# Kernel optimization log

Hardware: AMD Instinct MI355X
Metric: run time of the kernel (lower is better)

Reference implementation:

```python
import jax, jax.numpy as jnp
import numpy as np

B, D, E, H, O, TOP_K = 65536, 256, 16, 256, 256, 2
GATE_T = 1.0  # gate_temperature default


def setup_inputs() -> dict:
    key = jax.random.key(0)
    ks = jax.random.split(key, 8)
    sn = lambda k, shape, sc: (jax.random.normal(k, shape, jnp.float32) * sc)
    return {
        "x": sn(ks[0], (B, D), 1.0),
        # per-expert input bias, init N(0, 0.02) as in the module
        "bias": sn(ks[1], (E, D), 0.02),
        # expert MLP params: Linear(D,H) -> ReLU -> Linear(H,O), stacked over experts
        "W1": sn(ks[2], (E, D, H), 1.0 / np.sqrt(D)),
        "b1": jnp.zeros((E, H), jnp.float32),
        "W2": sn(ks[3], (E, H, O), 1.0 / np.sqrt(H)),
        "b2": jnp.zeros((E, O), jnp.float32),
        # gate MLP: Linear(D,4D) -> ReLU -> Linear(4D,D) -> ReLU -> Linear(D,E)
        "g1": sn(ks[4], (D, 4 * D), 1.0 / np.sqrt(D)),
        "gb1": jnp.zeros((4 * D,), jnp.float32),
        "g2": sn(ks[5], (4 * D, D), 1.0 / np.sqrt(4 * D)),
        "gb2": jnp.zeros((D,), jnp.float32),
        "g3": sn(ks[6], (D, E), 1.0 / np.sqrt(D)),
        "gb3": jnp.zeros((E,), jnp.float32),
    }


def reference(x, bias, W1, b1, W2, b2, g1, gb1, g2, gb2, g3, gb3):
    # --- gate ---
    h = jax.nn.relu(x @ g1 + gb1)
    h = jax.nn.relu(h @ g2 + gb2)
    gate_logits = h @ g3 + gb3              # [B, E]
    T = max(GATE_T, 1e-6)
    p = jax.nn.softmax(gate_logits / T, axis=1)

    # --- top-k sparsification + renormalize (top_k < num_experts) ---
    topv, topi = jax.lax.top_k(p, TOP_K)    # [B, K]
    rows = jnp.arange(p.shape[0])[:, None]
    p_sparse = jnp.zeros_like(p).at[rows, topi].set(topv)
    p = p_sparse / (p_sparse.sum(axis=1, keepdims=True) + 1e-9)

    # --- dense all-experts compute (module runs every expert on every token) ---
    xb = x[:, None, :] + bias[None]                                  # [B, E, D]
    he = jax.nn.relu(jnp.einsum("bed,edh->beh", xb, W1) + b1)      # [B, E, H]
    outs_all = jnp.einsum("beh,eho->beo", he, W2) + b2             # [B, E, O]

    # --- weighted combine (stopgrad_gate=False -> grads flow through p) ---
    y = jnp.einsum("be,beo->bo", p, outs_all)                      # [B, O]
    return (y, p)
```

## Files before the change

### kernel.cpp

```cpp
#include <hip/hip_runtime.h>
#include <cstdint>
#include <cstddef>

#define BTOK 65536
#define DDIM 256
#define NEXP 16
#define HDIM 256
#define ODIM 256
#define TAU2 1.2e-2f
#define TAU3 1.2e-4
#define AMB2_CAP 12288
#define AMB3_CAP 1024
#define LCAP (BTOK + 2048)

typedef _Float16 fp16x8 __attribute__((ext_vector_type(8)));
typedef float    f32x4_t __attribute__((ext_vector_type(4)));

__device__ __forceinline__ void async_ld16(const void* g, void* l) {
  __builtin_amdgcn_global_load_lds(
      (const __attribute__((address_space(1))) unsigned int*)g,
      (__attribute__((address_space(3))) unsigned int*)l, 16, 0, 0);
}

__global__ __launch_bounds__(256) void k_transpose_cvt(
    const float* __restrict__ src, _Float16* __restrict__ dhi,
    _Float16* __restrict__ dlo, int R, int C) {
  __shared__ float s[32][33];
  int bz = blockIdx.z;
  size_t stride = (size_t)R * C;
  src += (size_t)bz * stride;
  dhi += (size_t)bz * stride;
  if (dlo) dlo += (size_t)bz * stride;
  int c0 = blockIdx.x * 32, r0 = blockIdx.y * 32;
  int tx = threadIdx.x & 31, ty = threadIdx.x >> 5;
  for (int k = 0; k < 32; k += 8)
    s[ty + k][tx] = src[(size_t)(r0 + ty + k) * C + c0 + tx];
  __syncthreads();
  for (int k = 0; k < 32; k += 8) {
    float v = s[tx][ty + k];
    _Float16 h = (_Float16)v;
    size_t o = (size_t)(c0 + ty + k) * R + r0 + tx;
    dhi[o] = h;
    if (dlo) dlo[o] = (_Float16)(v - (float)h);
  }
}

__global__ __launch_bounds__(256) void k_xcvt_hi(const float* __restrict__ x,
                                                 _Float16* __restrict__ xhi, int n8) {
  int i = blockIdx.x * 256 + threadIdx.x;
  if (i >= n8) return;
  const float4* p = (const float4*)x;
  float4 a = p[(size_t)i * 2], b = p[(size_t)i * 2 + 1];
  float v[8] = {a.x, a.y, a.z, a.w, b.x, b.y, b.z, b.w};
  fp16x8 hv;
#pragma unroll
  for (int j = 0; j < 8; j++) hv[j] = (_Float16)v[j];
  *(fp16x8*)(xhi + (size_t)i * 8) = hv;
}

__global__ __launch_bounds__(256) void k_gemm_f16(
    const _Float16* __restrict__ A, const _Float16* __restrict__ B,
    const float* __restrict__ bias, _Float16* __restrict__ C,
    int M, int N, int K) {
  __shared__ _Float16 sA[128 * 32], sB[128 * 32];
  const int tid = threadIdx.x;
  const int lane = tid & 63;
  const int wave = tid >> 6;
  const int wr = wave >> 1, wc = wave & 1;
  const int m0 = blockIdx.y * 128, n0 = blockIdx.x * 128;
  f32x4_t zero4 = {0.f, 0.f, 0.f, 0.f};
  f32x4_t acc[4][4];
#pragma unroll
  for (int i = 0; i < 4; i++)
#pragma unroll
    for (int j = 0; j < 4; j++) acc[i][j] = zero4;

  for (int k0 = 0; k0 < K; k0 += 32) {
#pragma unroll
    for (int r = 0; r < 2; r++) {
      int idx = r * 256 + tid;
      int row = idx >> 2, ch = idx & 3;
      int gch = ch ^ (row & 3);
      async_ld16(A + (size_t)(m0 + row) * K + k0 + gch * 8, &sA[idx * 8]);
      async_ld16(B + (size_t)(n0 + row) * K + k0 + gch * 8, &sB[idx * 8]);
    }
    __syncthreads();
    fp16x8 a[4], b[4];
    int kc = lane >> 4;
#pragma unroll
    for (int i = 0; i < 4; i++) {
      int ar = wr * 64 + i * 16 + (lane & 15);
      a[i] = *(const fp16x8*)&sA[ar * 32 + ((kc ^ (ar & 3)) << 3)];
      int br = wc * 64 + i * 16 + (lane & 15);
      b[i] = *(const fp16x8*)&sB[br * 32 + ((kc ^ (br & 3)) << 3)];
    }
#pragma unroll
    for (int i = 0; i < 4; i++)
#pragma unroll
      for (int j = 0; j < 4; j++)
        acc[i][j] = __builtin_amdgcn_mfma_f32_16x16x32_f16(a[i], b[j], acc[i][j], 0, 0, 0);
    __syncthreads();
  }
#pragma unroll
  for (int j = 0; j < 4; j++) {
    int col = n0 + wc * 64 + j * 16 + (lane & 15);
    float bc = bias[col];
#pragma unroll
    for (int i = 0; i < 4; i++)
#pragma unroll
      for (int q = 0; q < 4; q++) {
        int row = m0 + wr * 64 + i * 16 + ((lane >> 4) << 2) + q;
        float v = acc[i][j][q] + bc;
        v = v > 0.f ? v : 0.f;
        C[(size_t)row * N + col] = (_Float16)v;
      }
  }
}

__global__ __launch_bounds__(256) void k_gemm_split(
    const _Float16* __restrict__ Ahi, const _Float16* __restrict__ Alo,
    const _Float16* __restrict__ Bhi, const _Float16* __restrict__ Blo,
    const float* __restrict__ bias,
    _Float16* __restrict__ Chi, _Float16* __restrict__ Clo,
    int M, int N, int K, const int* __restrict__ nAct) {
  int nA = *nAct;
  if (nA > M) nA = M;
  const int m0 = blockIdx.y * 128, n0 = blockIdx.x * 128;
  if (m0 >= nA) return;
  __shared__ _Float16 sAh[128 * 32], sAl[128 * 32], sBh[128 * 32], sBl[128 * 32];
  const int tid = threadIdx.x;
  const int lane = tid & 63;
  const int wave = tid >> 6;
  const int wr = wave >> 1, wc = wave & 1;
  f32x4_t zero4 = {0.f, 0.f, 0.f, 0.f};
  f32x4_t acc[4][4];
#pragma unroll
  for (int i = 0; i < 4; i++)
#pragma unroll
    for (int j = 0; j < 4; j++) acc[i][j] = zero4;

  for (int k0 = 0; k0 < K; k0 += 32) {
#pragma unroll
    for (int r = 0; r < 2; r++) {
      int idx = r * 256 + tid;
      int row = idx >> 2, ch = idx & 3;
      int gch = ch ^ (row & 3);
      size_t ga = (size_t)(m0 + row) * K + k0 + gch * 8;
      size_t gb = (size_t)(n0 + row) * K + k0 + gch * 8;
      async_ld16(Ahi + ga, &sAh[idx * 8]);
      async_ld16(Alo + ga, &sAl[idx * 8]);
      async_ld16(Bhi + gb, &sBh[idx * 8]);
      async_ld16(Blo + gb, &sBl[idx * 8]);
    }
    __syncthreads();
    fp16x8 ah[4], al[4], bh[4], bl[4];
    int kc = lane >> 4;
#pragma unroll
    for (int i = 0; i < 4; i++) {
      int ar = wr * 64 + i * 16 + (lane & 15);
      int offa = ar * 32 + ((kc ^ (ar & 3)) << 3);
      ah[i] = *(const fp16x8*)&sAh[offa];
      al[i] = *(const fp16x8*)&sAl[offa];
      int br = wc * 64 + i * 16 + (lane & 15);
      int offb = br * 32 + ((kc ^ (br & 3)) << 3);
      bh[i] = *(const fp16x8*)&sBh[offb];
      bl[i] = *(const fp16x8*)&sBl[offb];
    }
#pragma unroll
    for (int i = 0; i < 4; i++)
#pragma unroll
      for (int j = 0; j < 4; j++) {
        acc[i][j] = __builtin_amdgcn_mfma_f32_16x16x32_f16(ah[i], bh[j], acc[i][j], 0, 0, 0);
        acc[i][j] = __builtin_amdgcn_mfma_f32_16x16x32_f16(ah[i], bl[j], acc[i][j], 0, 0, 0);
        acc[i][j] = __builtin_amdgcn_mfma_f32_16x16x32_f16(al[i], bh[j], acc[i][j], 0, 0, 0);
      }
    __syncthreads();
  }
#pragma unroll
  for (int j = 0; j < 4; j++) {
    int col = n0 + wc * 64 + j * 16 + (lane & 15);
    float bc = bias[col];
#pragma unroll
    for (int i = 0; i < 4; i++)
#pragma unroll
      for (int q = 0; q < 4; q++) {
        int row = m0 + wr * 64 + i * 16 + ((lane >> 4) << 2) + q;
        float v = acc[i][j][q] + bc;
        v = v > 0.f ? v : 0.f;
        _Float16 h = (_Float16)v;
        size_t o = (size_t)row * N + col;
        Chi[o] = h;
        Clo[o] = (_Float16)(v - (float)h);
      }
  }
}

__global__ __launch_bounds__(256) void k_gate3_fast(
    const _Float16* __restrict__ h2h, const float* __restrict__ g3,
    const float* __restrict__ gb3,
    float* __restrict__ pout, int* __restrict__ idx0, int* __restrict__ idx1,
    float* __restrict__ w0, float* __restrict__ w1,
    int* __restrict__ amb2Cnt, int* __restrict__ amb2List,
    int* __restrict__ cnt0, int* __restrict__ cnt1) {
  __shared__ _Float16 shh[16 * 256];
  __shared__ float sg3[16][260];
  __shared__ float sgb[16];
  __shared__ float slog[16][17];
  __shared__ int sidx[16][2];
  __shared__ float swv[16][2];
  __shared__ int hc0[16], hc1[16];
  int tid = threadIdx.x;
  int tokBase = blockIdx.x * 16;
  if (tid < 16) { hc0[tid] = 0; hc1[tid] = 0; }
  {
    int t = tid >> 4, c = (tid & 15) * 16;
    size_t g = (size_t)(tokBase + t) * 256 + c;
    *(fp16x8*)&shh[t * 256 + c] = *(const fp16x8*)&h2h[g];
    *(fp16x8*)&shh[t * 256 + c + 8] = *(const fp16x8*)&h2h[g + 8];
  }
#pragma unroll
  for (int r = 0; r < 16; r++) {
    int j = r * 256 + tid;
    sg3[j & 15][j >> 4] = g3[j];
  }
  if (tid < 16) sgb[tid] = gb3[tid];
  __syncthreads();
  int t = tid >> 4, e = tid & 15;
  const _Float16* ph = &shh[t * 256];
  const float* pg = &sg3[e][0];
  float acc = 0.f;
  for (int k = 0; k < 256; k += 8) {
    fp16x8 hv = *(const fp16x8*)&ph[k];
    float4 ga = *(const float4*)&pg[k];
    float4 gb = *(const float4*)&pg[k + 4];
    acc = fmaf((float)hv[0], ga.x, acc);
    acc = fmaf((float)hv[1], ga.y, acc);
    acc = fmaf((float)hv[2], ga.z, acc);
    acc = fmaf((float)hv[3], ga.w, acc);
    acc = fmaf((float)hv[4], gb.x, acc);
    acc = fmaf((float)hv[5], gb.y, acc);
    acc = fmaf((float)hv[6], gb.z, acc);
    acc = fmaf((float)hv[7], gb.w, acc);
  }
  acc += sgb[e];
  slog[t][e] = acc;
  __syncthreads();
  if (e == 0) {
    float l[16];
#pragma unroll
    for (int i = 0; i < 16; i++) l[i] = slog[t][i];
    int i1 = 0;
    for (int i = 1; i < 16; i++) if (l[i] > l[i1]) i1 = i;
    int i2 = -1;
    for (int i = 0; i < 16; i++) { if (i == i1) continue; if (i2 < 0 || l[i] > l[i2]) i2 = i; }
    float l3 = -1e30f;
    for (int i = 0; i < 16; i++) { if (i == i1 || i == i2) continue; if (l[i] > l3) l3 = l[i]; }
    float lmax = l[i1];
    float S = 0.f;
    for (int i = 0; i < 16; i++) S += expf(l[i] - lmax);
    float p1 = 1.0f / S, p2 = expf(l[i2] - lmax) / S;
    float den = p1 + p2 + 1e-9f;
    sidx[t][0] = i1; sidx[t][1] = i2;
    swv[t][0] = p1 / den; swv[t][1] = p2 / den;
    atomicAdd(&hc0[i1], 1);
    atomicAdd(&hc1[i2], 1);
    if (l[i2] - l3 < TAU2) {
      int pos = atomicAdd(amb2Cnt, 1);
      if (pos < AMB2_CAP) amb2List[pos] = tokBase + t;
    }
  }
  __syncthreads();
  int i1 = sidx[t][0], i2 = sidx[t][1];
  float pv = (e == i1) ? swv[t][0] : ((e == i2) ? swv[t][1] : 0.f);
  pout[(size_t)(tokBase + t) * 16 + e] = pv;
  if (e == 0) {
    int tok = tokBase + t;
    idx0[tok] = i1; idx1[tok] = i2;
    w0[tok] = swv[t][0]; w1[tok] = swv[t][1];
  }
  if (tid < 16) {
    if (hc0[tid]) atomicAdd(&cnt0[tid], hc0[tid]);
    if (hc1[tid]) atomicAdd(&cnt1[tid], hc1[tid]);
  }
}

__global__ __launch_bounds__(256) void k_gather2(
    const float* __restrict__ x, const int* __restrict__ cnt,
    const int* __restrict__ list,
    _Float16* __restrict__ xgh, _Float16* __restrict__ xgl) {
  int n = *cnt; if (n > AMB2_CAP) n = AMB2_CAP;
  int s = blockIdx.x * 8 + (threadIdx.x >> 5);
  if (s >= n) return;
  int tok = list[s];
  int c = (threadIdx.x & 31) * 8;
  const float4* p = (const float4*)&x[(size_t)tok * 256 + c];
  float4 a = p[0], b = p[1];
  float v[8] = {a.x, a.y, a.z, a.w, b.x, b.y, b.z, b.w};
  fp16x8 hv, lv;
#pragma unroll
  for (int j = 0; j < 8; j++) {
    _Float16 h = (_Float16)v[j];
    hv[j] = h;
    lv[j] = (_Float16)(v[j] - (float)h);
  }
  *(fp16x8*)&xgh[(size_t)s * 256 + c] = hv;
  *(fp16x8*)&xgl[(size_t)s * 256 + c] = lv;
}

__global__ __launch_bounds__(256) void k_gate3_precise(
    const _Float16* __restrict__ h2ghi, const _Float16* __restrict__ h2glo,
    const float* __restrict__ g3, const float* __restrict__ gb3,
    const int* __restrict__ amb2Cnt, const int* __restrict__ amb2List,
    float* __restrict__ pout, int* __restrict__ idx0, int* __restrict__ idx1,
    float* __restrict__ w0, float* __restrict__ w1,
    int* __restrict__ amb3Cnt, int* __restrict__ amb3List,
    int* __restrict__ cnt0, int* __restrict__ cnt1) {
  __shared__ _Float16 shh[16 * 256], shl[16 * 256];
  __shared__ float sg3[16][260];
  __shared__ float sgb[16];
  __shared__ double slog[16][17];
  __shared__ int sidx[16][2];
  __shared__ float swv[16][2];
  int tid = threadIdx.x;
  int slotBase = blockIdx.x * 16;
  int n2 = *amb2Cnt; if (n2 > AMB2_CAP) n2 = AMB2_CAP;
  {
    int t = tid >> 4, c = (tid & 15) * 16;
    size_t g = (size_t)(slotBase + t) * 256 + c;
    *(fp16x8*)&shh[t * 256 + c] = *(const fp16x8*)&h2ghi[g];
    *(fp16x8*)&shh[t * 256 + c + 8] = *(const fp16x8*)&h2ghi[g + 8];
    *(fp16x8*)&shl[t * 256 + c] = *(const fp16x8*)&h2glo[g];
    *(fp16x8*)&shl[t * 256 + c + 8] = *(const fp16x8*)&h2glo[g + 8];
  }
#pragma unroll
  for (int r = 0; r < 16; r++) {
    int j = r * 256 + tid;
    sg3[j & 15][j >> 4] = g3[j];
  }
  if (tid < 16) sgb[tid] = gb3[tid];
  __syncthreads();
  int t = tid >> 4, e = tid & 15;
  int slot = slotBase + t;
  const _Float16* ph = &shh[t * 256];
  const _Float16* pl = &shl[t * 256];
  const float* pg = &sg3[e][0];
  double acc = 0.0;
  for (int k = 0; k < 256; k += 4) {
#pragma unroll
    for (int j = 0; j < 4; j++) {
      double a = (double)(float)ph[k + j] + (double)(float)pl[k + j];
      acc = fma(a, (double)pg[k + j], acc);
    }
  }
  acc += (double)sgb[e];
  slog[t][e] = acc;
  __syncthreads();
  if (e == 0 && slot < n2) {
    int tok = amb2List[slot];
    double l[16];
#pragma unroll
    for (int i = 0; i < 16; i++) l[i] = slog[t][i];
    int i1 = 0;
    for (int i = 1; i < 16; i++) if (l[i] > l[i1]) i1 = i;
    int i2 = -1;
    for (int i = 0; i < 16; i++) { if (i == i1) continue; if (i2 < 0 || l[i] > l[i2]) i2 = i; }
    double l3 = -1e300;
    for (int i = 0; i < 16; i++) { if (i == i1 || i == i2) continue; if (l[i] > l3) l3 = l[i]; }
    double lmax = l[i1];
    double S = 0.0;
    for (int i = 0; i < 16; i++) S += exp(l[i] - lmax);
    double p1 = 1.0 / S, p2 = exp(l[i2] - lmax) / S;
    double den = p1 + p2 + 1e-9;
    sidx[t][0] = i1; sidx[t][1] = i2;
    swv[t][0] = (float)(p1 / den); swv[t][1] = (float)(p2 / den);
    int o0 = idx0[tok], o1 = idx1[tok];
    if (i1 != o0) { atomicSub(&cnt0[o0], 1); atomicAdd(&cnt0[i1], 1); }
    if (i2 != o1) { atomicSub(&cnt1[o1], 1); atomicAdd(&cnt1[i2], 1); }
    if (l[i2] - l3 < TAU3) {
      int pos = atomicAdd(amb3Cnt, 1);
      if (pos < AMB3_CAP) amb3List[pos] = tok;
    }
  }
  __syncthreads();
  if (slot < n2) {
    int tok = amb2List[slot];
    int i1 = sidx[t][0], i2 = sidx[t][1];
    float pv = (e == i1) ? swv[t][0] : ((e == i2) ? swv[t][1] : 0.f);
    pout[(size_t)tok * 16 + e] = pv;
    if (e == 0) {
      idx0[tok] = i1; idx1[tok] = i2;
      w0[tok] = swv[t][0]; w1[tok] = swv[t][1];
    }
  }
}

__global__ __launch_bounds__(256) void k_ref_l1(
    const float* __restrict__ x, const float* __restrict__ g1,
    const float* __restrict__ gb1,
    const int* __restrict__ cnt, const int* __restrict__ list,
    double* __restrict__ h1d) {
  int n = *cnt; if (n > AMB3_CAP) n = AMB3_CAP;
  int t = blockIdx.y;
  if (t >= n) return;
  __shared__ float sx[256];
  __shared__ double sred[4][64];
  int tid = threadIdx.x;
  int tok = list[t];
  sx[tid] = x[(size_t)tok * 256 + tid];
  __syncthreads();
  int o = tid & 63, p = tid >> 6;
  int out = blockIdx.x * 64 + o;
  double a = 0.0;
  const float* gp = g1 + (size_t)(p * 64) * 1024 + out;
  const float* xp = &sx[p * 64];
#pragma unroll 8
  for (int k = 0; k < 64; k++)
    a = fma((double)xp[k], (double)gp[(size_t)k * 1024], a);
  sred[p][o] = a;
  __syncthreads();
  if (p == 0) {
    double s = sred[0][o] + sred[1][o] + sred[2][o] + sred[3][o] + (double)gb1[out];
    h1d[(size_t)t * 1024 + out] = s > 0.0 ? s : 0.0;
  }
}

__global__ __launch_bounds__(512) void k_ref_l2(
    const double* __restrict__ h1d, const float* __restrict__ g2,
    const float* __restrict__ gb2,
    const int* __restrict__ cnt, double* __restrict__ h2d) {
  int n = *cnt; if (n > AMB3_CAP) n = AMB3_CAP;
  int t = blockIdx.y;
  if (t >= n) return;
  __shared__ double sh1[1024];
  __shared__ double sred[8][64];
  int tid = threadIdx.x;
  sh1[tid] = h1d[(size_t)t * 1024 + tid];
  sh1[512 + tid] = h1d[(size_t)t * 1024 + 512 + tid];
  __syncthreads();
  int o = tid & 63, p = tid >> 6;
  int out = blockIdx.x * 64 + o;
  double a = 0.0;
  const float* gp = g2 + (size_t)(p * 128) * 256 + out;
  const double* hp = &sh1[p * 128];
#pragma unroll 4
  for (int k = 0; k < 128; k++)
    a = fma(hp[k], (double)gp[(size_t)k * 256], a);
  sred[p][o] = a;
  __syncthreads();
  if (p == 0) {
    double s = sred[0][o] + sred[1][o] + sred[2][o] + sred[3][o] +
               sred[4][o] + sred[5][o] + sred[6][o] + sred[7][o] + (double)gb2[out];
    h2d[(size_t)t * 256 + out] = s > 0.0 ? s : 0.0;
  }
}

__global__ __launch_bounds__(256) void k_ref_l3(
    const double* __restrict__ h2d, const float* __restrict__ g3,
    const float* __restrict__ gb3,
    const int* __restrict__ cnt, const int* __restrict__ list,
    float* __restrict__ pout, int* __restrict__ idx0, int* __restrict__ idx1,
    float* __restrict__ w0, float* __restrict__ w1,
    int* __restrict__ cnt0, int* __restrict__ cnt1) {
  int n = *cnt; if (n > AMB3_CAP) n = AMB3_CAP;
  int t = blockIdx.x;
  if (t >= n) return;
  __shared__ double sh2[256];
  __shared__ double sl16[16][17];
  __shared__ int sidx[2];
  __shared__ float swv[2];
  int tid = threadIdx.x;
  int tok = list[t];
  sh2[tid] = h2d[(size_t)t * 256 + tid];
  __syncthreads();
  {
    int o = tid & 15, pp = tid >> 4;
    double a = 0.0;
#pragma unroll
    for (int k = pp * 16; k < pp * 16 + 16; k++)
      a = fma(sh2[k], (double)g3[(size_t)k * 16 + o], a);
    sl16[pp][o] = a;
  }
  __syncthreads();
  if (tid == 0) {
    double l[16];
    for (int o = 0; o < 16; o++) {
      double a = (double)gb3[o];
      for (int p = 0; p < 16; p++) a += sl16[p][o];
      l[o] = a;
    }
    int i1 = 0;
    for (int i = 1; i < 16; i++) if (l[i] > l[i1]) i1 = i;
    int i2 = -1;
    for (int i = 0; i < 16; i++) { if (i == i1) continue; if (i2 < 0 || l[i] > l[i2]) i2 = i; }
    double lmax = l[i1];
    double S = 0.0;
    for (int i = 0; i < 16; i++) S += exp(l[i] - lmax);
    double p1 = 1.0 / S, p2 = exp(l[i2] - lmax) / S;
    double den = p1 + p2 + 1e-9;
    float fw0 = (float)(p1 / den), fw1 = (float)(p2 / den);
    int o0 = idx0[tok], o1 = idx1[tok];
    if (i1 != o0) { atomicSub(&cnt0[o0], 1); atomicAdd(&cnt0[i1], 1); }
    if (i2 != o1) { atomicSub(&cnt1[o1], 1); atomicAdd(&cnt1[i2], 1); }
    sidx[0] = i1; sidx[1] = i2;
    swv[0] = fw0; swv[1] = fw1;
    idx0[tok] = i1; idx1[tok] = i2;
    w0[tok] = fw0; w1[tok] = fw1;
  }
  __syncthreads();
  if (tid < 16) {
    float pv = (tid == sidx[0]) ? swv[0] : ((tid == sidx[1]) ? swv[1] : 0.f);
    pout[(size_t)tok * 16 + tid] = pv;
  }
}

__global__ void k_offsets(const int* __restrict__ cnt0, const int* __restrict__ cnt1,
                          int* off0, int* off1, int* cur0, int* cur1,
                          int* dExpC, int* dRowC, int* nTiles) {
  if (threadIdx.x == 0) {
    int tot = 0, nt = 0;
    for (int e = 0; e < 16; e++) {
      off0[e] = tot; cur0[e] = 0;
      int tiles = (cnt0[e] + 127) >> 7;
      for (int ti = 0; ti < tiles; ti++) { dExpC[nt] = e; dRowC[nt] = tot + ti * 128; nt++; }
      tot += tiles * 128;
    }
    nTiles[0] = nt;
    tot = 0;
    for (int e = 0; e < 16; e++) {
      off1[e] = tot; cur1[e] = 0;
      int tiles = (cnt1[e] + 127) >> 7;
      for (int ti = 0; ti < tiles; ti++) { dExpC[nt] = e; dRowC[nt] = LCAP + tot + ti * 128; nt++; }
      tot += tiles * 128;
    }
    nTiles[1] = nt;
  }
}

__global__ __launch_bounds__(256) void k_scatter(
    const int* __restrict__ idx0, const int* __restrict__ idx1,
    const float* __restrict__ w0, const float* __restrict__ w1,
    const int* __restrict__ off0, const int* __restrict__ off1,
    int* cur0, int* cur1,
    int* __restrict__ tok0, float* __restrict__ wl0,
    int* __restrict__ tok1, float* __restrict__ wl1) {
  __shared__ int c0[16], c1[16], b0[16], b1[16];
  int tid = threadIdx.x;
  if (tid < 16) { c0[tid] = 0; c1[tid] = 0; }
  __syncthreads();
  int b = blockIdx.x * 256 + tid;
  int e0 = idx0[b], e1 = idx1[b];
  int r0 = atomicAdd(&c0[e0], 1);
  int r1 = atomicAdd(&c1[e1], 1);
  __syncthreads();
  if (tid < 16) { b0[tid] = atomicAdd(&cur0[tid], c0[tid]); b1[tid] = atomicAdd(&cur1[tid], c1[tid]); }
  __syncthreads();
  int p0 = off0[e0] + b0[e0] + r0;
  tok0[p0] = b; wl0[p0] = w0[b];
  int p1 = off1[e1] + b1[e1] + r1;
  tok1[p1] = b; wl1[p1] = w1[b];
}

__global__ __launch_bounds__(512) void k_grp_l1(
    const _Float16* __restrict__ xhi, const float* __restrict__ bias,
    const _Float16* __restrict__ W1T, const float* __restrict__ b1,
    const int* __restrict__ tokAll,
    const int* __restrict__ dExp, const int* __restrict__ dRow,
    const int* __restrict__ nT, _Float16* __restrict__ heg) {
  __shared__ _Float16 sA[128 * 32];
  __shared__ _Float16 sB[256 * 32];
  __shared__ int sTok[128];
  __shared__ float sBias[256];
  int tid = threadIdx.x, lane = tid & 63, wave = tid >> 6;
  int wr = wave >> 2, wc = wave & 3;
  f32x4_t zero4 = {0.f, 0.f, 0.f, 0.f};
  int nt = *nT;
  for (int t = blockIdx.x; t < nt; t += gridDim.x) {
    int e = dExp[t], rowOff = dRow[t];
    if (tid < 128) sTok[tid] = tokAll[rowOff + tid];
    if (tid < 256) sBias[tid] = bias[e * 256 + tid];
    __syncthreads();
    f32x4_t acc[4][4];
#pragma unroll
    for (int i = 0; i < 4; i++)
#pragma unroll
      for (int j = 0; j < 4; j++) acc[i][j] = zero4;
    const _Float16* W1e = W1T + (size_t)e * 65536;
    for (int k0 = 0; k0 < 256; k0 += 32) {
      {
        int row = tid >> 2, ch = tid & 3, gch = ch ^ (row & 3);
        int tok = sTok[row];
        int tk = tok < 0 ? 0 : tok;
        fp16x8 v = *(const fp16x8*)&xhi[(size_t)tk * 256 + k0 + gch * 8];
        const float* bp = &sBias[k0 + gch * 8];
#pragma unroll
        for (int j = 0; j < 8; j++) v[j] = (_Float16)((float)v[j] + bp[j]);
        *(fp16x8*)&sA[tid * 8] = v;
      }
#pragma unroll
      for (int r = 0; r < 2; r++) {
        int idx = r * 512 + tid;
        int row = idx >> 2, ch = idx & 3, gch = ch ^ (row & 3);
        async_ld16(W1e + (size_t)row * 256 + k0 + gch * 8, &sB[idx * 8]);
      }
      __syncthreads();
      fp16x8 a[4], b[4];
      int kc = lane >> 4;
#pragma unroll
      for (int i = 0; i < 4; i++) {
        int ar = wr * 64 + i * 16 + (lane & 15);
        a[i] = *(const fp16x8*)&sA[ar * 32 + ((kc ^ (ar & 3)) << 3)];
        int br = wc * 64 + i * 16 + (lane & 15);
        b[i] = *(const fp16x8*)&sB[br * 32 + ((kc ^ (br & 3)) << 3)];
      }
#pragma unroll
      for (int i = 0; i < 4; i++)
#pragma unroll
        for (int j = 0; j < 4; j++)
          acc[i][j] = __builtin_amdgcn_mfma_f32_16x16x32_f16(a[i], b[j], acc[i][j], 0, 0, 0);
      __syncthreads();
    }
#pragma unroll
    for (int j = 0; j < 4; j++) {
      int col = wc * 64 + j * 16 + (lane & 15);
      float bb = b1[e * 256 + col];
#pragma unroll
      for (int i = 0; i < 4; i++)
#pragma unroll
        for (int q = 0; q < 4; q++) {
          int row = wr * 64 + i * 16 + ((lane >> 4) << 2) + q;
          float v = acc[i][j][q] + bb;
          heg[(size_t)(rowOff + row) * 256 + col] = (_Float16)(v > 0.f ? v : 0.f);
        }
    }
    __syncthreads();
  }
}

template <int PASSB>
__global__ __launch_bounds__(512) void k_grp_l2(
    const _Float16* __restrict__ heg, const _Float16* __restrict__ W2T,
    const float* __restrict__ b2,
    const int* __restrict__ tokAll, const float* __restrict__ wlAll,
    const int* __restrict__ dExp, const int* __restrict__ dRow,
    const int* __restrict__ nT0, const int* __restrict__ nTC,
    float* __restrict__ y) {
  __shared__ _Float16 sA[128 * 32];
  __shared__ _Float16 sB[256 * 32];
  __shared__ int sTok[128];
  __shared__ float sW[128];
  int tid = threadIdx.x, lane = tid & 63, wave = tid >> 6;
  int wr = wave >> 2, wc = wave & 3;
  f32x4_t zero4 = {0.f, 0.f, 0.f, 0.f};
  int tStart = PASSB ? *nT0 : 0;
  int tEnd = PASSB ? *nTC : *nT0;
  for (int t = tStart + blockIdx.x; t < tEnd; t += gridDim.x) {
    int e = dExp[t], rowOff = dRow[t];
    if (tid < 128) { sTok[tid] = tokAll[rowOff + tid]; sW[tid] = wlAll[rowOff + tid]; }
    __syncthreads();
    f32x4_t acc[4][4];
#pragma unroll
    for (int i = 0; i < 4; i++)
#pragma unroll
      for (int j = 0; j < 4; j++) acc[i][j] = zero4;
    const _Float16* W2e = W2T + (size_t)e * 65536;
    for (int k0 = 0; k0 < 256; k0 += 32) {
      {
        int row = tid >> 2, ch = tid & 3, gch = ch ^ (row & 3);
        async_ld16(heg + (size_t)(rowOff + row) * 256 + k0 + gch * 8, &sA[tid * 8]);
      }
#pragma unroll
      for (int r = 0; r < 2; r++) {
        int idx = r * 512 + tid;
        int row = idx >> 2, ch = idx & 3, gch = ch ^ (row & 3);
        async_ld16(W2e + (size_t)row * 256 + k0 + gch * 8, &sB[idx * 8]);
      }
      __syncthreads();
      fp16x8 a[4], b[4];
      int kc = lane >> 4;
#pragma unroll
      for (int i = 0; i < 4; i++) {
        int ar = wr * 64 + i * 16 + (lane & 15);
        a[i] = *(const fp16x8*)&sA[ar * 32 + ((kc ^ (ar & 3)) << 3)];
        int br = wc * 64 + i * 16 + (lane & 15);
        b[i] = *(const fp16x8*)&sB[br * 32 + ((kc ^ (br & 3)) << 3)];
      }
#pragma unroll
      for (int i = 0; i < 4; i++)
#pragma unroll
        for (int j = 0; j < 4; j++)
          acc[i][j] = __builtin_amdgcn_mfma_f32_16x16x32_f16(a[i], b[j], acc[i][j], 0, 0, 0);
      __syncthreads();
    }
#pragma unroll
    for (int j = 0; j < 4; j++) {
      int col = wc * 64 + j * 16 + (lane & 15);
      float bb = b2[e * 256 + col];
#pragma unroll
      for (int i = 0; i < 4; i++)
#pragma unroll
        for (int q = 0; q < 4; q++) {
          int row = wr * 64 + i * 16 + ((lane >> 4) << 2) + q;
          int tok = sTok[row];
          if (tok >= 0) {
            float v = (acc[i][j][q] + bb) * sW[row];
            size_t o = (size_t)tok * 256 + col;
            if (PASSB) y[o] += v; else y[o] = v;
          }
        }
    }
    __syncthreads();
  }
}

extern "C" void kernel_launch(void* const* d_in, const int* in_sizes, int n_in,
                              void* d_out, int out_size, void* d_ws, size_t ws_size,
                              hipStream_t stream) {
  const float* x   = (const float*)d_in[0];
  const float* bias= (const float*)d_in[1];
  const float* W1  = (const float*)d_in[2];
  const float* b1  = (const float*)d_in[3];
  const float* W2  = (const float*)d_in[4];
  const float* b2  = (const float*)d_in[5];
  const float* g1  = (const float*)d_in[6];
  const float* gb1 = (const float*)d_in[7];
  const float* g2  = (const float*)d_in[8];
  const float* gb2 = (const float*)d_in[9];
  const float* g3  = (const float*)d_in[10];
  const float* gb3 = (const float*)d_in[11];
  float* y    = (float*)d_out;
  float* pout = y + (size_t)BTOK * 256;

  char* w = (char*)d_ws;
  auto alloc = [&](size_t bytes) -> char* {
    char* p = w;
    w += (bytes + 255) & ~(size_t)255;
    return p;
  };
  _Float16* xhi  = (_Float16*)alloc((size_t)BTOK * 256 * 2);
  _Float16* h2h  = (_Float16*)alloc((size_t)BTOK * 256 * 2);
  _Float16* g1Th = (_Float16*)alloc((size_t)256 * 1024 * 2);
  _Float16* g1Tl = (_Float16*)alloc((size_t)256 * 1024 * 2);
  _Float16* g2Th = (_Float16*)alloc((size_t)256 * 1024 * 2);
  _Float16* g2Tl = (_Float16*)alloc((size_t)256 * 1024 * 2);
  _Float16* W1T  = (_Float16*)alloc((size_t)16 * 65536 * 2);
  _Float16* W2T  = (_Float16*)alloc((size_t)16 * 65536 * 2);
  int*   idx0 = (int*)alloc((size_t)BTOK * 4);
  int*   idx1 = (int*)alloc((size_t)BTOK * 4);
  float* w0a  = (float*)alloc((size_t)BTOK * 4);
  float* w1a  = (float*)alloc((size_t)BTOK * 4);
  int*   ctrl = (int*)alloc(4096);
  int*   amb2List = (int*)alloc((size_t)AMB2_CAP * 4);
  int*   amb3List = (int*)alloc((size_t)AMB3_CAP * 4);
  int*   dExpC = (int*)alloc(1088 * 4);
  int*   dRowC = (int*)alloc(1088 * 4);
  int*   tokAll = (int*)alloc((size_t)2 * LCAP * 4);
  float* wlAll  = (float*)alloc((size_t)2 * LCAP * 4);
  _Float16* xgh  = (_Float16*)alloc((size_t)AMB2_CAP * 256 * 2);
  _Float16* xgl  = (_Float16*)alloc((size_t)AMB2_CAP * 256 * 2);
  _Float16* h1gh = (_Float16*)alloc((size_t)AMB2_CAP * 1024 * 2);
  _Float16* h1gl = (_Float16*)alloc((size_t)AMB2_CAP * 1024 * 2);
  _Float16* h2gh = (_Float16*)alloc((size_t)AMB2_CAP * 256 * 2);
  _Float16* h2gl = (_Float16*)alloc((size_t)AMB2_CAP * 256 * 2);
  _Float16* heg = (_Float16*)xgh;
  double* h1d = (double*)alloc((size_t)AMB3_CAP * 1024 * 8);
  double* h2d = (double*)alloc((size_t)AMB3_CAP * 256 * 8);

  size_t used = (size_t)(w - (char*)d_ws);
  size_t remain = ws_size > used ? ws_size - used : 0;
  int CG = 1;
  while (CG < 64 && (size_t)(BTOK / CG) * 1024 * 2 + 1024 > remain) CG <<= 1;
  int MC = BTOK / CG;
  _Float16* h1h = (_Float16*)alloc((size_t)MC * 1024 * 2);

  int* cnt0 = ctrl + 0;  int* cnt1 = ctrl + 16;
  int* off0 = ctrl + 32; int* off1 = ctrl + 48;
  int* cur0 = ctrl + 64; int* cur1 = ctrl + 80;
  int* nTiles = ctrl + 96;
  int* amb2Cnt = ctrl + 112;
  int* amb3Cnt = ctrl + 116;

  hipMemsetAsync(ctrl, 0, 4096, stream);
  hipMemsetAsync(tokAll, 0xFF, (size_t)2 * LCAP * 4, stream);

  dim3 tb(256);
  k_transpose_cvt<<<dim3(32, 8, 1), tb, 0, stream>>>(g1, g1Th, g1Tl, 256, 1024);
  k_transpose_cvt<<<dim3(8, 32, 1), tb, 0, stream>>>(g2, g2Th, g2Tl, 1024, 256);
  k_transpose_cvt<<<dim3(8, 8, 16), tb, 0, stream>>>(W1, W1T, nullptr, 256, 256);
  k_transpose_cvt<<<dim3(8, 8, 16), tb, 0, stream>>>(W2, W2T, nullptr, 256, 256);
  k_xcvt_hi<<<(BTOK * 256 / 8 + 255) / 256, tb, 0, stream>>>(x, xhi, BTOK * 256 / 8);

  for (int c = 0; c < CG; c++) {
    const _Float16* xh = xhi + (size_t)c * MC * 256;
    k_gemm_f16<<<dim3(8, MC / 128), tb, 0, stream>>>(xh, g1Th, gb1, h1h, MC, 1024, 256);
    k_gemm_f16<<<dim3(2, MC / 128), tb, 0, stream>>>(h1h, g2Th, gb2,
                                                     h2h + (size_t)c * MC * 256, MC, 256, 1024);
  }
  k_gate3_fast<<<BTOK / 16, tb, 0, stream>>>(h2h, g3, gb3, pout, idx0, idx1,
                                             w0a, w1a, amb2Cnt, amb2List, cnt0, cnt1);

  k_gather2<<<AMB2_CAP / 8, tb, 0, stream>>>(x, amb2Cnt, amb2List, xgh, xgl);
  k_gemm_split<<<dim3(8, AMB2_CAP / 128), tb, 0, stream>>>(
      xgh, xgl, g1Th, g1Tl, gb1, h1gh, h1gl, AMB2_CAP, 1024, 256, amb2Cnt);
  k_gemm_split<<<dim3(2, AMB2_CAP / 128), tb, 0, stream>>>(
      h1gh, h1gl, g2Th, g2Tl, gb2, h2gh, h2gl, AMB2_CAP, 256, 1024, amb2Cnt);
  k_gate3_precise<<<AMB2_CAP / 16, tb, 0, stream>>>(
      h2gh, h2gl, g3, gb3, amb2Cnt, amb2List, pout, idx0, idx1, w0a, w1a,
      amb3Cnt, amb3List, cnt0, cnt1);

  k_ref_l1<<<dim3(16, AMB3_CAP), tb, 0, stream>>>(x, g1, gb1, amb3Cnt, amb3List, h1d);
  k_ref_l2<<<dim3(4, AMB3_CAP), 512, 0, stream>>>(h1d, g2, gb2, amb3Cnt, h2d);
  k_ref_l3<<<AMB3_CAP, tb, 0, stream>>>(h2d, g3, gb3, amb3Cnt, amb3List,
                                        pout, idx0, idx1, w0a, w1a, cnt0, cnt1);

  k_offsets<<<1, 64, 0, stream>>>(cnt0, cnt1, off0, off1, cur0, cur1,
                                  dExpC, dRowC, nTiles);
  k_scatter<<<BTOK / 256, tb, 0, stream>>>(idx0, idx1, w0a, w1a, off0, off1,
                                           cur0, cur1, tokAll, wlAll,
                                           tokAll + LCAP, wlAll + LCAP);
  k_grp_l1<<<1056, 512, 0, stream>>>(xhi, bias, W1T, b1, tokAll,
                                     dExpC, dRowC, nTiles + 1, heg);
  k_grp_l2<0><<<528, 512, 0, stream>>>(heg, W2T, b2, tokAll, wlAll,
                                       dExpC, dRowC, nTiles, nTiles + 1, y);
  k_grp_l2<1><<<528, 512, 0, stream>>>(heg, W2T, b2, tokAll, wlAll,
                                       dExpC, dRowC, nTiles, nTiles + 1, y);
}
```

Before: 726.8 us.

## Use MFMA for gate logits, split top-2, and stage expert epilogues through LDS

The scalar FMA gate-3 kernel is replaced by an MFMA 16x16x32 fp16 logits kernel, using g3 converted to fp16, plus a separate one-token-per-thread top-2 kernel that goes through a global logits buffer. The expert layer-1 and layer-2 epilogues now stage outputs in shared memory so each row is written with vectorized, coalesced global stores instead of scattered scalar ones. This trades extra syncthreads and an extra logits round trip for fewer FP32 ALU operations and better store coalescing. Converting g3 to fp16 changes logit precision, which could shift which tokens are flagged as ambiguous and sent through the precise path.

```diff
diff --git a/kernel.cpp b/kernel.cpp
--- a/kernel.cpp
+++ b/kernel.cpp
@@ -43,6 +43,13 @@
     dhi[o] = h;
     if (dlo) dlo[o] = (_Float16)(v - (float)h);
   }
+}
+
+__global__ __launch_bounds__(256) void k_g3cvt(const float* __restrict__ g3,
+                                               _Float16* __restrict__ g3T) {
+  int idx = blockIdx.x * 256 + threadIdx.x;
+  int k = idx >> 4, e = idx & 15;
+  g3T[e * 256 + k] = (_Float16)g3[idx];
 }
 
 __global__ __launch_bounds__(256) void k_xcvt_hi(const float* __restrict__ x,
@@ -195,93 +202,98 @@
   }
 }
 
-__global__ __launch_bounds__(256) void k_gate3_fast(
-    const _Float16* __restrict__ h2h, const float* __restrict__ g3,
-    const float* __restrict__ gb3,
+__global__ __launch_bounds__(256) void k_logits(
+    const _Float16* __restrict__ h2h, const _Float16* __restrict__ g3T,
+    const float* __restrict__ gb3, float* __restrict__ logits) {
+  __shared__ _Float16 sA[128 * 32];
+  __shared__ _Float16 sG[16 * 264];
+  int tid = threadIdx.x, lane = tid & 63, wave = tid >> 6;
+  int m0 = blockIdx.x * 128;
+  {
+    int r = tid >> 4, c = (tid & 15) * 16;
+    *(fp16x8*)&sG[r * 264 + c]     = *(const fp16x8*)&g3T[r * 256 + c];
+    *(fp16x8*)&sG[r * 264 + c + 8] = *(const fp16x8*)&g3T[r * 256 + c + 8];
+  }
+  f32x4_t zero4 = {0.f, 0.f, 0.f, 0.f};
+  f32x4_t acc[2] = {zero4, zero4};
+  for (int k0 = 0; k0 < 256; k0 += 32) {
+#pragma unroll
+    for (int r = 0; r < 2; r++) {
+      int idx = r * 256 + tid;
+      int row = idx >> 2, ch = idx & 3, gch = ch ^ (row & 3);
+      async_ld16(h2h + (size_t)(m0 + row) * 256 + k0 + gch * 8, &sA[idx * 8]);
+    }
+    __syncthreads();
+    int kc = lane >> 4;
+    fp16x8 b = *(const fp16x8*)&sG[(lane & 15) * 264 + k0 + kc * 8];
+#pragma unroll
+    for (int i = 0; i < 2; i++) {
+      int ar = wave * 32 + i * 16 + (lane & 15);
+      fp16x8 a = *(const fp16x8*)&sA[ar * 32 + ((kc ^ (ar & 3)) << 3)];
+      acc[i] = __builtin_amdgcn_mfma_f32_16x16x32_f16(a, b, acc[i], 0, 0, 0);
+    }
+    __syncthreads();
+  }
+  float bb = gb3[lane & 15];
+#pragma unroll
+  for (int i = 0; i < 2; i++)
+#pragma unroll
+    for (int q = 0; q < 4; q++) {
+      int row = m0 + wave * 32 + i * 16 + ((lane >> 4) << 2) + q;
+      logits[(size_t)row * 16 + (lane & 15)] = acc[i][q] + bb;
+    }
+}
+
+__global__ __launch_bounds__(256) void k_top2(
+    const float* __restrict__ logits,
     float* __restrict__ pout, int* __restrict__ idx0, int* __restrict__ idx1,
     float* __restrict__ w0, float* __restrict__ w1,
     int* __restrict__ amb2Cnt, int* __restrict__ amb2List,
     int* __restrict__ cnt0, int* __restrict__ cnt1) {
-  __shared__ _Float16 shh[16 * 256];
-  __shared__ float sg3[16][260];
-  __shared__ float sgb[16];
-  __shared__ float slog[16][17];
-  __shared__ int sidx[16][2];
-  __shared__ float swv[16][2];
   __shared__ int hc0[16], hc1[16];
   int tid = threadIdx.x;
-  int tokBase = blockIdx.x * 16;
   if (tid < 16) { hc0[tid] = 0; hc1[tid] = 0; }
-  {
-    int t = tid >> 4, c = (tid & 15) * 16;
-    size_t g = (size_t)(tokBase + t) * 256 + c;
-    *(fp16x8*)&shh[t * 256 + c] = *(const fp16x8*)&h2h[g];
-    *(fp16x8*)&shh[t * 256 + c + 8] = *(const fp16x8*)&h2h[g + 8];
-  }
-#pragma unroll
-  for (int r = 0; r < 16; r++) {
-    int j = r * 256 + tid;
-    sg3[j & 15][j >> 4] = g3[j];
-  }
-  if (tid < 16) sgb[tid] = gb3[tid];
-  __syncthreads();
-  int t = tid >> 4, e = tid & 15;
-  const _Float16* ph = &shh[t * 256];
-  const float* pg = &sg3[e][0];
-  float acc = 0.f;
-  for (int k = 0; k < 256; k += 8) {
-    fp16x8 hv = *(const fp16x8*)&ph[k];
-    float4 ga = *(const float4*)&pg[k];
-    float4 gb = *(const float4*)&pg[k + 4];
-    acc = fmaf((float)hv[0], ga.x, acc);
-    acc = fmaf((float)hv[1], ga.y, acc);
-    acc = fmaf((float)hv[2], ga.z, acc);
-    acc = fmaf((float)hv[3], ga.w, acc);
-    acc = fmaf((float)hv[4], gb.x, acc);
-    acc = fmaf((float)hv[5], gb.y, acc);
-    acc = fmaf((float)hv[6], gb.z, acc);
-    acc = fmaf((float)hv[7], gb.w, acc);
-  }
-  acc += sgb[e];
-  slog[t][e] = acc;
-  __syncthreads();
-  if (e == 0) {
-    float l[16];
-#pragma unroll
-    for (int i = 0; i < 16; i++) l[i] = slog[t][i];
-    int i1 = 0;
-    for (int i = 1; i < 16; i++) if (l[i] > l[i1]) i1 = i;
-    int i2 = -1;
-    for (int i = 0; i < 16; i++) { if (i == i1) continue; if (i2 < 0 || l[i] > l[i2]) i2 = i; }
-    float l3 = -1e30f;
-    for (int i = 0; i < 16; i++) { if (i == i1 || i == i2) continue; if (l[i] > l3) l3 = l[i]; }
-    float lmax = l[i1];
-    float S = 0.f;
-    for (int i = 0; i < 16; i++) S += expf(l[i] - lmax);
-    float p1 = 1.0f / S, p2 = expf(l[i2] - lmax) / S;
-    float den = p1 + p2 + 1e-9f;
-    sidx[t][0] = i1; sidx[t][1] = i2;
-    swv[t][0] = p1 / den; swv[t][1] = p2 / den;
-    atomicAdd(&hc0[i1], 1);
-    atomicAdd(&hc1[i2], 1);
-    if (l[i2] - l3 < TAU2) {
-      int pos = atomicAdd(amb2Cnt, 1);
-      if (pos < AMB2_CAP) amb2List[pos] = tokBase + t;
-    }
-  }
-  __syncthreads();
-  int i1 = sidx[t][0], i2 = sidx[t][1];
-  float pv = (e == i1) ? swv[t][0] : ((e == i2) ? swv[t][1] : 0.f);
-  pout[(size_t)(tokBase + t) * 16 + e] = pv;
-  if (e == 0) {
-    int tok = tokBase + t;
-    idx0[tok] = i1; idx1[tok] = i2;
-    w0[tok] = swv[t][0]; w1[tok] = swv[t][1];
-  }
-  if (tid < 16) {
-    if (hc0[tid]) atomicAdd(&cnt0[tid], hc0[tid]);
-    if (hc1[tid]) atomicAdd(&cnt1[tid], hc1[tid]);
-  }
+  __syncthreads();
+  int tok = blockIdx.x * 256 + tid;
+  const float4* lp = (const float4*)&logits[(size_t)tok * 16];
+  float4 v0 = lp[0], v1 = lp[1], v2 = lp[2], v3 = lp[3];
+  float l[16] = {v0.x, v0.y, v0.z, v0.w, v1.x, v1.y, v1.z, v1.w,
+                 v2.x, v2.y, v2.z, v2.w, v3.x, v3.y, v3.z, v3.w};
+  float l1v = -1e30f; int i1 = -1;
+#pragma unroll
+  for (int e = 0; e < 16; e++) if (l[e] > l1v) { l1v = l[e]; i1 = e; }
+  float l2v = -1e30f; int i2 = -1;
+#pragma unroll
+  for (int e = 0; e < 16; e++) if (e != i1 && l[e] > l2v) { l2v = l[e]; i2 = e; }
+  float l3v = -1e30f;
+#pragma unroll
+  for (int e = 0; e < 16; e++) if (e != i1 && e != i2 && l[e] > l3v) l3v = l[e];
+  float S = 0.f;
+#pragma unroll
+  for (int e = 0; e < 16; e++) S += expf(l[e] - l1v);
+  float p1 = 1.0f / S, p2 = expf(l2v - l1v) / S;
+  float den = p1 + p2 + 1e-9f;
+  float W0 = p1 / den, W1v = p2 / den;
+  float4* po = (float4*)&pout[(size_t)tok * 16];
+#pragma unroll
+  for (int g = 0; g < 4; g++) {
+    float4 o;
+    o.x = (g * 4 + 0 == i1) ? W0 : ((g * 4 + 0 == i2) ? W1v : 0.f);
+    o.y = (g * 4 + 1 == i1) ? W0 : ((g * 4 + 1 == i2) ? W1v : 0.f);
+    o.z = (g * 4 + 2 == i1) ? W0 : ((g * 4 + 2 == i2) ? W1v : 0.f);
+    o.w = (g * 4 + 3 == i1) ? W0 : ((g * 4 + 3 == i2) ? W1v : 0.f);
+    po[g] = o;
+  }
+  idx0[tok] = i1; idx1[tok] = i2;
+  w0[tok] = W0; w1[tok] = W1v;
+  atomicAdd(&hc0[i1], 1);
+  atomicAdd(&hc1[i2], 1);
+  if (l2v - l3v < TAU2) {
+    int pos = atomicAdd(amb2Cnt, 1);
+    if (pos < AMB2_CAP) amb2List[pos] = tok;
+  }
+  __syncthreads();
+  if (tid < 16) { atomicAdd(&cnt0[tid], hc0[tid]); atomicAdd(&cnt1[tid], hc1[tid]); }
 }
 
 __global__ __launch_bounds__(256) void k_gather2(
@@ -570,6 +582,8 @@
   __shared__ _Float16 sB[256 * 32];
   __shared__ int sTok[128];
   __shared__ float sBias[256];
+  __shared__ float sB1c[256];
+  __shared__ _Float16 sOutH[16 * 268];
   int tid = threadIdx.x, lane = tid & 63, wave = tid >> 6;
   int wr = wave >> 2, wc = wave & 3;
   f32x4_t zero4 = {0.f, 0.f, 0.f, 0.f};
@@ -577,7 +591,7 @@
   for (int t = blockIdx.x; t < nt; t += gridDim.x) {
     int e = dExp[t], rowOff = dRow[t];
     if (tid < 128) sTok[tid] = tokAll[rowOff + tid];
-    if (tid < 256) sBias[tid] = bias[e * 256 + tid];
+    if (tid < 256) { sBias[tid] = bias[e * 256 + tid]; sB1c[tid] = b1[e * 256 + tid]; }
     __syncthreads();
     f32x4_t acc[4][4];
 #pragma unroll
@@ -620,17 +634,29 @@
       __syncthreads();
     }
 #pragma unroll
-    for (int j = 0; j < 4; j++) {
-      int col = wc * 64 + j * 16 + (lane & 15);
-      float bb = b1[e * 256 + col];
-#pragma unroll
-      for (int i = 0; i < 4; i++)
-#pragma unroll
-        for (int q = 0; q < 4; q++) {
-          int row = wr * 64 + i * 16 + ((lane >> 4) << 2) + q;
-          float v = acc[i][j][q] + bb;
-          heg[(size_t)(rowOff + row) * 256 + col] = (_Float16)(v > 0.f ? v : 0.f);
+    for (int wrg = 0; wrg < 2; wrg++) {
+#pragma unroll
+      for (int i = 0; i < 4; i++) {
+        __syncthreads();
+        if (wr == wrg) {
+#pragma unroll
+          for (int j = 0; j < 4; j++) {
+            float bb = sB1c[wc * 64 + j * 16 + (lane & 15)];
+#pragma unroll
+            for (int q = 0; q < 4; q++) {
+              int rowc = ((lane >> 4) << 2) + q;
+              float v = acc[i][j][q] + bb;
+              v = v > 0.f ? v : 0.f;
+              sOutH[rowc * 268 + wc * 64 + j * 16 + (lane & 15)] = (_Float16)v;
+            }
+          }
         }
+        __syncthreads();
+        int rowc = tid >> 5, seg = tid & 31;
+        int row128 = wrg * 64 + i * 16 + rowc;
+        fp16x8 hv = *(const fp16x8*)&sOutH[rowc * 268 + seg * 8];
+        *(fp16x8*)&heg[(size_t)(rowOff + row128) * 256 + seg * 8] = hv;
+      }
     }
     __syncthreads();
   }
@@ -648,6 +674,8 @@
   __shared__ _Float16 sB[256 * 32];
   __shared__ int sTok[128];
   __shared__ float sW[128];
+  __shared__ float sB2c[256];
+  __shared__ float sOut[16 * 266];
   int tid = threadIdx.x, lane = tid & 63, wave = tid >> 6;
   int wr = wave >> 2, wc = wave & 3;
   f32x4_t zero4 = {0.f, 0.f, 0.f, 0.f};
@@ -656,6 +684,7 @@
   for (int t = tStart + blockIdx.x; t < tEnd; t += gridDim.x) {
     int e = dExp[t], rowOff = dRow[t];
     if (tid < 128) { sTok[tid] = tokAll[rowOff + tid]; sW[tid] = wlAll[rowOff + tid]; }
+    if (tid < 256) sB2c[tid] = b2[e * 256 + tid];
     __syncthreads();
     f32x4_t acc[4][4];
 #pragma unroll
@@ -692,21 +721,41 @@
       __syncthreads();
     }
 #pragma unroll
-    for (int j = 0; j < 4; j++) {
-      int col = wc * 64 + j * 16 + (lane & 15);
-      float bb = b2[e * 256 + col];
-#pragma unroll
-      for (int i = 0; i < 4; i++)
-#pragma unroll
-        for (int q = 0; q < 4; q++) {
-          int row = wr * 64 + i * 16 + ((lane >> 4) << 2) + q;
-          int tok = sTok[row];
-          if (tok >= 0) {
-            float v = (acc[i][j][q] + bb) * sW[row];
-            size_t o = (size_t)tok * 256 + col;
-            if (PASSB) y[o] += v; else y[o] = v;
+    for (int wrg = 0; wrg < 2; wrg++) {
+#pragma unroll
+      for (int i = 0; i < 4; i++) {
+        __syncthreads();
+        if (wr == wrg) {
+#pragma unroll
+          for (int j = 0; j < 4; j++) {
+            float bb = sB2c[wc * 64 + j * 16 + (lane & 15)];
+#pragma unroll
+            for (int q = 0; q < 4; q++) {
+              int rowc = ((lane >> 4) << 2) + q;
+              int row128 = wrg * 64 + i * 16 + rowc;
+              sOut[rowc * 266 + wc * 64 + j * 16 + (lane & 15)] =
+                  (acc[i][j][q] + bb) * sW[row128];
+            }
           }
         }
+        __syncthreads();
+        int rowc = tid >> 5, seg = tid & 31;
+        int row128 = wrg * 64 + i * 16 + rowc;
+        int tok = sTok[row128];
+        if (tok >= 0) {
+          float4 v0 = *(const float4*)&sOut[rowc * 266 + seg * 8];
+          float4 v1 = *(const float4*)&sOut[rowc * 266 + seg * 8 + 4];
+          float* yp = &y[(size_t)tok * 256 + seg * 8];
+          if (PASSB) {
+            float4 o0 = *(const float4*)yp;
+            float4 o1 = *(const float4*)(yp + 4);
+            v0.x += o0.x; v0.y += o0.y; v0.z += o0.z; v0.w += o0.w;
+            v1.x += o1.x; v1.y += o1.y; v1.z += o1.z; v1.w += o1.w;
+          }
+          *(float4*)yp = v0;
+          *(float4*)(yp + 4) = v1;
+        }
+      }
     }
     __syncthreads();
   }
@@ -742,8 +791,10 @@
   _Float16* g1Tl = (_Float16*)alloc((size_t)256 * 1024 * 2);
   _Float16* g2Th = (_Float16*)alloc((size_t)256 * 1024 * 2);
   _Float16* g2Tl = (_Float16*)alloc((size_t)256 * 1024 * 2);
+  _Float16* g3Th = (_Float16*)alloc((size_t)16 * 256 * 2);
   _Float16* W1T  = (_Float16*)alloc((size_t)16 * 65536 * 2);
   _Float16* W2T  = (_Float16*)alloc((size_t)16 * 65536 * 2);
+  float* logits = (float*)alloc((size_t)BTOK * 16 * 4);
   int*   idx0 = (int*)alloc((size_t)BTOK * 4);
   int*   idx1 = (int*)alloc((size_t)BTOK * 4);
   float* w0a  = (float*)alloc((size_t)BTOK * 4);
@@ -787,6 +838,7 @@
   k_transpose_cvt<<<dim3(8, 32, 1), tb, 0, stream>>>(g2, g2Th, g2Tl, 1024, 256);
   k_transpose_cvt<<<dim3(8, 8, 16), tb, 0, stream>>>(W1, W1T, nullptr, 256, 256);
   k_transpose_cvt<<<dim3(8, 8, 16), tb, 0, stream>>>(W2, W2T, nullptr, 256, 256);
+  k_g3cvt<<<16, tb, 0, stream>>>(g3, g3Th);
   k_xcvt_hi<<<(BTOK * 256 / 8 + 255) / 256, tb, 0, stream>>>(x, xhi, BTOK * 256 / 8);
 
   for (int c = 0; c < CG; c++) {
@@ -795,8 +847,9 @@
     k_gemm_f16<<<dim3(2, MC / 128), tb, 0, stream>>>(h1h, g2Th, gb2,
                                                      h2h + (size_t)c * MC * 256, MC, 256, 1024);
   }
-  k_gate3_fast<<<BTOK / 16, tb, 0, stream>>>(h2h, g3, gb3, pout, idx0, idx1,
-                                             w0a, w1a, amb2Cnt, amb2List, cnt0, cnt1);
+  k_logits<<<BTOK / 128, tb, 0, stream>>>(h2h, g3Th, gb3, logits);
+  k_top2<<<BTOK / 256, tb, 0, stream>>>(logits, pout, idx0, idx1, w0a, w1a,
+                                        amb2Cnt, amb2List, cnt0, cnt1);
 
   k_gather2<<<AMB2_CAP / 8, tb, 0, stream>>>(x, amb2Cnt, amb2List, xgh, xgl);
   k_gemm_split<<<dim3(8, AMB2_CAP / 128), tb, 0, stream>>>(
```

New measurement: 648.7 us. 10.8% less time.
